# Kernel optimization log

Hardware: AMD Instinct MI355X
Metric: run time of the kernel (lower is better)

## Reference

```python
import jax, jax.numpy as jnp
import numpy as np


def setup_inputs() -> dict:
    key = jax.random.key(0)
    k0, k1 = jax.random.split(key)
    b, n, m, e = 8, 2048, 2048, 1024
    mat_0 = jax.random.normal(k0, (b, n, e), dtype=jnp.float32)
    mat_1 = jax.random.normal(k1, (b, m, e), dtype=jnp.float32)
    return {"mat_0": mat_0, "mat_1": mat_1}


def reference(mat_0, mat_1):
    # Original tiles to [b,n,m,e], multiplies, and sums over e.
    # Mathematically identical to a batched QK^T matmul: [b,n,m].
    return jnp.einsum('bne,bme->bnm', mat_0, mat_1)
```

## Files before the change

kernel.cpp:

```cpp
#include <hip/hip_runtime.h>
#include <hip/hip_bf16.h>

typedef __attribute__((ext_vector_type(8))) short short8;
typedef __attribute__((ext_vector_type(4))) float f32x4;
typedef __attribute__((ext_vector_type(4))) unsigned int u32x4;
typedef unsigned short u16;
typedef __attribute__((address_space(1))) void gvoid;
typedef __attribute__((address_space(3))) void lvoid;

static constexpr int BATCH = 8;
static constexpr int NDIM  = 2048;
static constexpr int MDIM  = 2048;
static constexpr int EDIM  = 1024;

__device__ __forceinline__ unsigned bf16rne_pair(float a, float b) {
  unsigned ua = __float_as_uint(a), ub = __float_as_uint(b);
  ua = (ua + 0x7FFFu + ((ua >> 16) & 1u)) >> 16;
  ub = (ub + 0x7FFFu + ((ub >> 16) & 1u)) >> 16;
  return ua | (ub << 16);
}

__global__ __launch_bounds__(256)
void cvt_kernel(const float* __restrict__ A, const float* __restrict__ B,
                u16* __restrict__ Abf, u16* __restrict__ Bbf) {
  const int half = (BATCH * NDIM * EDIM) / (256 * 8);
  int bid = blockIdx.x;
  const float* src; u16* dst;
  if (bid < half) { src = A; dst = Abf; }
  else            { src = B; dst = Bbf; bid -= half; }
  size_t idx = ((size_t)bid * 256 + threadIdx.x) * 8;
  f32x4 x = *(const f32x4*)(src + idx);
  f32x4 y = *(const f32x4*)(src + idx + 4);
  u32x4 r;
  r[0] = bf16rne_pair(x[0], x[1]);
  r[1] = bf16rne_pair(x[2], x[3]);
  r[2] = bf16rne_pair(y[0], y[1]);
  r[3] = bf16rne_pair(y[2], y[3]);
  *(u32x4*)(dst + idx) = r;
}

__device__ __forceinline__ void async_cp16(const void* g, void* l) {
  __builtin_amdgcn_global_load_lds((gvoid*)g, (lvoid*)l, 16, 0, 0);
}

#define BAR() do { asm volatile("" ::: "memory"); \
                   __builtin_amdgcn_s_barrier(); \
                   asm volatile("" ::: "memory"); } while (0)
#define WAITVM(N) asm volatile("s_waitcnt vmcnt(" #N ")" ::: "memory")

static constexpr int BM = 256;
static constexpr int BN = 256;
static constexpr int BK = 64;
static constexpr int KTILES = EDIM / BK;

__global__ __launch_bounds__(512, 2)
void bmm_8ph_kernel(const u16* __restrict__ A, const u16* __restrict__ B,
                    float* __restrict__ C) {
  __shared__ u16 sh[2][2][BM * BK];

  const int tid  = threadIdx.x;
  const int lane = tid & 63;
  const int wave = tid >> 6;
  const int wr   = wave >> 2;
  const int wc   = wave & 3;
  const int quad = lane >> 4;
  const int ml   = lane & 15;

  const int tcol  = blockIdx.x;
  const int trow  = blockIdx.y;
  const int batch = blockIdx.z;

  const u16* Ab = A + (size_t)batch * NDIM * EDIM + (size_t)trow * BM * EDIM;
  const u16* Bb = B + (size_t)batch * MDIM * EDIM + (size_t)tcol * BN * EDIM;

  const int r0 = tid >> 3;
  const int cs = (tid & 7) ^ (r0 & 7);
  const u16* gA = Ab + (size_t)r0 * EDIM + cs * 8;
  const u16* gB = Bb + (size_t)r0 * EDIM + cs * 8;

#define STG(buf, ab, h, gptr, t) do {                                          \
    const u16* _g = (gptr) + (size_t)((h) * 128) * EDIM + (size_t)(t) * BK;    \
    async_cp16(_g,                   &sh[buf][ab][(h) * 8192 + wave * 512]);   \
    async_cp16(_g + (size_t)64 * EDIM,                                         \
               &sh[buf][ab][(h) * 8192 + 4096 + wave * 512]);                  \
  } while (0)

  const int aBase = (wr * 128 + ml) * 64;
  const int bBase = (wc * 64 + ml) * 64;
  const int kc0 = ((quad     ) ^ (ml & 7)) * 8;
  const int kc1 = ((quad + 4 ) ^ (ml & 7)) * 8;

  short8 ar[4][2], br0[2][2], br1[2][2];
  f32x4 acc[8][4] = {};

#define LDA(buf, mh) do {                                                      \
    _Pragma("unroll")                                                          \
    for (int q = 0; q < 4; ++q) {                                              \
      ar[q][0] = *(const short8*)&sh[buf][0][aBase + (mh)*4096 + q*1024 + kc0];\
      ar[q][1] = *(const short8*)&sh[buf][0][aBase + (mh)*4096 + q*1024 + kc1];\
    } } while (0)

#define LDB(dst, buf, nh) do {                                                 \
    _Pragma("unroll")                                                          \
    for (int n = 0; n < 2; ++n) {                                              \
      dst[n][0] = *(const short8*)&sh[buf][1][bBase + (nh)*2048 + n*1024 + kc0];\
      dst[n][1] = *(const short8*)&sh[buf][1][bBase + (nh)*2048 + n*1024 + kc1];\
    } } while (0)

#define MM(mh, nh, BSRC) do {                                                  \
    __builtin_amdgcn_s_setprio(1);                                             \
    _Pragma("unroll")                                                          \
    for (int q = 0; q < 4; ++q)                                                \
      _Pragma("unroll")                                                        \
      for (int n = 0; n < 2; ++n)                                              \
        _Pragma("unroll")                                                      \
        for (int ks = 0; ks < 2; ++ks)                                         \
          acc[(mh)*4 + q][(nh)*2 + n] = __builtin_amdgcn_mfma_f32_16x16x32_bf16(\
              ar[q][ks], BSRC[n][ks], acc[(mh)*4 + q][(nh)*2 + n], 0, 0, 0);   \
    __builtin_amdgcn_s_setprio(0);                                             \
  } while (0)

  STG(0, 0, 0, gA, 0);
  STG(0, 0, 1, gA, 0);
  STG(0, 1, 0, gB, 0);
  STG(0, 1, 1, gB, 0);
  STG(1, 1, 0, gB, 1);
  STG(1, 1, 1, gB, 1);
  WAITVM(4);
  BAR();

#pragma unroll 1
  for (int i = 0; i < 7; ++i) {
    const int t1 = 2 * i + 1, p0 = 2 * i + 2, p1 = 2 * i + 3;
    LDA(0, 0); LDB(br0, 0, 0);
    STG(1, 0, 0, gA, t1);
    BAR(); MM(0, 0, br0); BAR();
    LDB(br1, 0, 1);
    STG(1, 0, 1, gA, t1);
    BAR(); MM(0, 1, br1); BAR();
    LDA(0, 1);
    STG(0, 1, 0, gB, p0);
    BAR(); MM(1, 1, br1); BAR();
    STG(0, 1, 1, gB, p0);
    WAITVM(4);
    BAR(); MM(1, 0, br0); BAR();
    LDA(1, 0); LDB(br0, 1, 0);
    STG(0, 0, 0, gA, p0);
    BAR(); MM(0, 0, br0); BAR();
    LDB(br1, 1, 1);
    STG(0, 0, 1, gA, p0);
    BAR(); MM(0, 1, br1); BAR();
    LDA(1, 1);
    STG(1, 1, 0, gB, p1);
    BAR(); MM(1, 1, br1); BAR();
    STG(1, 1, 1, gB, p1);
    WAITVM(4);
    BAR(); MM(1, 0, br0); BAR();
  }

  {
    LDA(0, 0); LDB(br0, 0, 0);
    STG(1, 0, 0, gA, 15);
    BAR(); MM(0, 0, br0); BAR();
    LDB(br1, 0, 1);
    STG(1, 0, 1, gA, 15);
    BAR(); MM(0, 1, br1); BAR();
    LDA(0, 1);
    BAR(); MM(1, 1, br1); BAR();
    WAITVM(0);
    BAR(); MM(1, 0, br0); BAR();
    LDA(1, 0); LDB(br0, 1, 0);
    BAR(); MM(0, 0, br0); BAR();
    LDB(br1, 1, 1);
    BAR(); MM(0, 1, br1); BAR();
    LDA(1, 1);
    BAR(); MM(1, 1, br1); BAR();
    MM(1, 0, br0);
  }

  float* Cb = C + (size_t)batch * NDIM * MDIM
                + (size_t)(trow * BM + wr * 128 + quad * 4) * MDIM
                + (tcol * BN + wc * 64 + ml);
#pragma unroll
  for (int mi = 0; mi < 8; ++mi) {
#pragma unroll
    for (int ni = 0; ni < 4; ++ni) {
      float* cp = Cb + (size_t)(mi * 16) * MDIM + ni * 16;
#pragma unroll
      for (int r = 0; r < 4; ++r)
        cp[(size_t)r * MDIM] = acc[mi][ni][r];
    }
  }
#undef STG
#undef LDA
#undef LDB
#undef MM
}

static constexpr int FBM = 128;
static constexpr int FBN = 128;
static constexpr int FBK = 32;
static constexpr int FKIT = EDIM / FBK;
static constexpr int LSTR = 40;

__device__ __forceinline__ unsigned pk(float lo, float hi) {
  return __builtin_amdgcn_perm(__float_as_uint(hi), __float_as_uint(lo), 0x07060302u);
}
__device__ __forceinline__ u32x4 pack8(f32x4 x, f32x4 y) {
  u32x4 r;
  r[0] = pk(x[0], x[1]); r[1] = pk(x[2], x[3]);
  r[2] = pk(y[0], y[1]); r[3] = pk(y[2], y[3]);
  return r;
}

__global__ __launch_bounds__(256, 3)
void bmm_bt_kernel(const float* __restrict__ A, const float* __restrict__ B,
                   float* __restrict__ C) {
  __shared__ u16 As[FBM * LSTR];
  __shared__ u16 Bs[FBN * LSTR];

  const int tid  = threadIdx.x;
  const int lane = tid & 63;
  const int wave = tid >> 6;
  const int quad = lane >> 4;
  const int ml   = lane & 15;
  const int wrow = (wave >> 1) * 64;
  const int wcol = (wave & 1) * 64;

  const int tcol  = blockIdx.x;
  const int trow  = blockIdx.y;
  const int batch = blockIdx.z;

  const float* Ab = A + (size_t)batch * NDIM * EDIM + (size_t)trow * FBM * EDIM;
  const float* Bb = B + (size_t)batch * MDIM * EDIM + (size_t)tcol * FBN * EDIM;
  float*       Cb = C + (size_t)batch * NDIM * MDIM;

  const int r0 = tid >> 2;
  const int p0 = (tid & 3) * 8;
  const int r1 = r0 + 64;

  const float* pA0 = Ab + (size_t)r0 * EDIM + p0;
  const float* pA1 = Ab + (size_t)r1 * EDIM + p0;
  const float* pB0 = Bb + (size_t)r0 * EDIM + p0;
  const float* pB1 = Bb + (size_t)r1 * EDIM + p0;

  u16* wA0 = &As[r0 * LSTR + p0];
  u16* wA1 = &As[r1 * LSTR + p0];
  u16* wB0 = &Bs[r0 * LSTR + p0];
  u16* wB1 = &Bs[r1 * LSTR + p0];

  f32x4 a0 = *(const f32x4*)(pA0);
  f32x4 a1 = *(const f32x4*)(pA0 + 4);
  f32x4 a2 = *(const f32x4*)(pA1);
  f32x4 a3 = *(const f32x4*)(pA1 + 4);
  f32x4 b0 = *(const f32x4*)(pB0);
  f32x4 b1 = *(const f32x4*)(pB0 + 4);
  f32x4 b2 = *(const f32x4*)(pB1);
  f32x4 b3 = *(const f32x4*)(pB1 + 4);

  f32x4 acc[4][4] = {};

  for (int kb = 0; kb < FKIT; ++kb) {
    __syncthreads();
    *(u32x4*)wA0 = pack8(a0, a1);
    *(u32x4*)wA1 = pack8(a2, a3);
    *(u32x4*)wB0 = pack8(b0, b1);
    *(u32x4*)wB1 = pack8(b2, b3);
    __syncthreads();

    if (kb + 1 < FKIT) {
      const int off = (kb + 1) * FBK;
      a0 = *(const f32x4*)(pA0 + off);
      a1 = *(const f32x4*)(pA0 + off + 4);
      a2 = *(const f32x4*)(pA1 + off);
      a3 = *(const f32x4*)(pA1 + off + 4);
      b0 = *(const f32x4*)(pB0 + off);
      b1 = *(const f32x4*)(pB0 + off + 4);
      b2 = *(const f32x4*)(pB1 + off);
      b3 = *(const f32x4*)(pB1 + off + 4);
    }

    short8 af[4], bfr[4];
#pragma unroll
    for (int i = 0; i < 4; ++i)
      af[i] = *(const short8*)&As[(wrow + i * 16 + ml) * LSTR + quad * 8];
#pragma unroll
    for (int i = 0; i < 4; ++i)
      bfr[i] = *(const short8*)&Bs[(wcol + i * 16 + ml) * LSTR + quad * 8];

#pragma unroll
    for (int mi = 0; mi < 4; ++mi)
#pragma unroll
      for (int ni = 0; ni < 4; ++ni)
        acc[mi][ni] = __builtin_amdgcn_mfma_f32_16x16x32_bf16(
            af[mi], bfr[ni], acc[mi][ni], 0, 0, 0);
  }

  const int crow = trow * FBM + wrow + quad * 4;
  const int ccol = tcol * FBN + wcol + ml;
#pragma unroll
  for (int mi = 0; mi < 4; ++mi) {
#pragma unroll
    for (int ni = 0; ni < 4; ++ni) {
      float* cp = Cb + (size_t)(crow + mi * 16) * MDIM + (ccol + ni * 16);
#pragma unroll
      for (int r = 0; r < 4; ++r)
        cp[(size_t)r * MDIM] = acc[mi][ni][r];
    }
  }
}

extern "C" void kernel_launch(void* const* d_in, const int* in_sizes, int n_in,
                              void* d_out, int out_size, void* d_ws, size_t ws_size,
                              hipStream_t stream) {
  const float* A = (const float*)d_in[0];
  const float* B = (const float*)d_in[1];
  float*       C = (float*)d_out;

  const size_t elems = (size_t)BATCH * NDIM * EDIM;
  const size_t need  = 2 * elems * sizeof(u16);

  if (ws_size >= need) {
    u16* Abf = (u16*)d_ws;
    u16* Bbf = Abf + elems;
    const int cvt_blocks = (int)(2 * elems / (256 * 8));
    cvt_kernel<<<cvt_blocks, 256, 0, stream>>>(A, B, Abf, Bbf);
    dim3 grid(MDIM / BN, NDIM / BM, BATCH);
    bmm_8ph_kernel<<<grid, dim3(512), 0, stream>>>(Abf, Bbf, C);
  } else {
    dim3 grid(MDIM / FBN, NDIM / FBM, BATCH);
    bmm_bt_kernel<<<grid, dim3(256), 0, stream>>>(A, B, C);
  }
}
```

Measured before the change: 288.9 us.

## Fuse fp32-to-bf16 conversion into GEMM staging and remap blocks for locality

Drops the separate conversion pass and its bf16 workspace. The GEMM now loads fp32 tiles from global memory into registers, packs them with the hardware bf16 convert instruction, and writes them swizzled into LDS, interleaved with the existing 8-phase MFMA schedule. It also remaps block indices so that consecutive workgroups are spread across batches and tiles. This removes a full read and write of both inputs plus one kernel launch. In exchange, each workgroup reads twice as many bytes from global memory through registers instead of async LDS loads, which raises register pressure and adds lgkm waits to every phase.

Result: slower. 525.9 us (+82.0%).

```diff
diff --git a/kernel.cpp b/kernel.cpp
--- a/kernel.cpp
+++ b/kernel.cpp
@@ -1,61 +1,26 @@
 #include <hip/hip_runtime.h>
-#include <hip/hip_bf16.h>
 
 typedef __attribute__((ext_vector_type(8))) short short8;
 typedef __attribute__((ext_vector_type(4))) float f32x4;
-typedef __attribute__((ext_vector_type(4))) unsigned int u32x4;
+typedef __attribute__((ext_vector_type(2))) unsigned int u32x2;
 typedef unsigned short u16;
-typedef __attribute__((address_space(1))) void gvoid;
-typedef __attribute__((address_space(3))) void lvoid;
 
 static constexpr int BATCH = 8;
 static constexpr int NDIM  = 2048;
 static constexpr int MDIM  = 2048;
 static constexpr int EDIM  = 1024;
-
-__device__ __forceinline__ unsigned bf16rne_pair(float a, float b) {
-  unsigned ua = __float_as_uint(a), ub = __float_as_uint(b);
-  ua = (ua + 0x7FFFu + ((ua >> 16) & 1u)) >> 16;
-  ub = (ub + 0x7FFFu + ((ub >> 16) & 1u)) >> 16;
-  return ua | (ub << 16);
-}
-
-__global__ __launch_bounds__(256)
-void cvt_kernel(const float* __restrict__ A, const float* __restrict__ B,
-                u16* __restrict__ Abf, u16* __restrict__ Bbf) {
-  const int half = (BATCH * NDIM * EDIM) / (256 * 8);
-  int bid = blockIdx.x;
-  const float* src; u16* dst;
-  if (bid < half) { src = A; dst = Abf; }
-  else            { src = B; dst = Bbf; bid -= half; }
-  size_t idx = ((size_t)bid * 256 + threadIdx.x) * 8;
-  f32x4 x = *(const f32x4*)(src + idx);
-  f32x4 y = *(const f32x4*)(src + idx + 4);
-  u32x4 r;
-  r[0] = bf16rne_pair(x[0], x[1]);
-  r[1] = bf16rne_pair(x[2], x[3]);
-  r[2] = bf16rne_pair(y[0], y[1]);
-  r[3] = bf16rne_pair(y[2], y[3]);
-  *(u32x4*)(dst + idx) = r;
-}
-
-__device__ __forceinline__ void async_cp16(const void* g, void* l) {
-  __builtin_amdgcn_global_load_lds((gvoid*)g, (lvoid*)l, 16, 0, 0);
-}
+static constexpr int BM    = 256;
+static constexpr int BN    = 256;
+static constexpr int BK    = 64;
 
 #define BAR() do { asm volatile("" ::: "memory"); \
                    __builtin_amdgcn_s_barrier(); \
                    asm volatile("" ::: "memory"); } while (0)
-#define WAITVM(N) asm volatile("s_waitcnt vmcnt(" #N ")" ::: "memory")
-
-static constexpr int BM = 256;
-static constexpr int BN = 256;
-static constexpr int BK = 64;
-static constexpr int KTILES = EDIM / BK;
+#define WFENCE() asm volatile("s_waitcnt lgkmcnt(0)" ::: "memory")
 
 __global__ __launch_bounds__(512, 2)
-void bmm_8ph_kernel(const u16* __restrict__ A, const u16* __restrict__ B,
-                    float* __restrict__ C) {
+void bmm_fused_kernel(const float* __restrict__ A, const float* __restrict__ B,
+                      float* __restrict__ C) {
   __shared__ u16 sh[2][2][BM * BK];
 
   const int tid  = threadIdx.x;
@@ -66,109 +31,139 @@
   const int quad = lane >> 4;
   const int ml   = lane & 15;
 
-  const int tcol  = blockIdx.x;
-  const int trow  = blockIdx.y;
-  const int batch = blockIdx.z;
-
-  const u16* Ab = A + (size_t)batch * NDIM * EDIM + (size_t)trow * BM * EDIM;
-  const u16* Bb = B + (size_t)batch * MDIM * EDIM + (size_t)tcol * BN * EDIM;
-
-  const int r0 = tid >> 3;
-  const int cs = (tid & 7) ^ (r0 & 7);
-  const u16* gA = Ab + (size_t)r0 * EDIM + cs * 8;
-  const u16* gB = Bb + (size_t)r0 * EDIM + cs * 8;
-
-#define STG(buf, ab, h, gptr, t) do {                                          \
-    const u16* _g = (gptr) + (size_t)((h) * 128) * EDIM + (size_t)(t) * BK;    \
-    async_cp16(_g,                   &sh[buf][ab][(h) * 8192 + wave * 512]);   \
-    async_cp16(_g + (size_t)64 * EDIM,                                         \
-               &sh[buf][ab][(h) * 8192 + 4096 + wave * 512]);                  \
-  } while (0)
+  const int flat  = (int)blockIdx.x + 8 * (int)blockIdx.y + 64 * (int)blockIdx.z;
+  const int nf    = (flat & 7) * 64 + (flat >> 3);
+  const int batch = nf >> 6;
+  const int trow  = (nf >> 3) & 7;
+  const int tcol  = nf & 7;
+
+  const float* Ab = A + (size_t)batch * NDIM * EDIM + (size_t)trow * BM * EDIM;
+  const float* Bb = B + (size_t)batch * MDIM * EDIM + (size_t)tcol * BN * EDIM;
+
+  const int rowb = tid >> 4;
+  const int colf = (tid & 15) * 4;
+  const int swzoff = ((((tid & 15) >> 1) ^ (rowb & 7)) << 3) | ((tid & 1) << 2);
+  const float* pA = Ab + (size_t)rowb * EDIM + colf;
+  const float* pB = Bb + (size_t)rowb * EDIM + colf;
 
   const int aBase = (wr * 128 + ml) * 64;
   const int bBase = (wc * 64 + ml) * 64;
-  const int kc0 = ((quad     ) ^ (ml & 7)) * 8;
-  const int kc1 = ((quad + 4 ) ^ (ml & 7)) * 8;
+  const int kc0 = ((quad    ) ^ (ml & 7)) * 8;
+  const int kc1 = ((quad + 4) ^ (ml & 7)) * 8;
 
   short8 ar[4][2], br0[2][2], br1[2][2];
   f32x4 acc[8][4] = {};
+  f32x4 s0v[4], s1v[4];
+
+#define ISS(Sp, P, h, t) do {                                                  \
+    const float* _p = (P) + (size_t)((h) * 128) * EDIM + (size_t)(t) * BK;     \
+    Sp[0] = *(const f32x4*)(_p);                                               \
+    Sp[1] = *(const f32x4*)(_p + (size_t)32 * EDIM);                           \
+    Sp[2] = *(const f32x4*)(_p + (size_t)64 * EDIM);                           \
+    Sp[3] = *(const f32x4*)(_p + (size_t)96 * EDIM);                           \
+  } while (0)
+
+#define WRT(Sp, buf, ab, h) do {                                               \
+    _Pragma("unroll")                                                          \
+    for (int _j = 0; _j < 4; ++_j) {                                           \
+      unsigned _lo, _hi;                                                       \
+      asm("v_cvt_pk_bf16_f32 %0, %1, %2"                                       \
+          : "=v"(_lo) : "v"(Sp[_j][0]), "v"(Sp[_j][1]));                       \
+      asm("v_cvt_pk_bf16_f32 %0, %1, %2"                                       \
+          : "=v"(_hi) : "v"(Sp[_j][2]), "v"(Sp[_j][3]));                       \
+      u32x2 _u; _u[0] = _lo; _u[1] = _hi;                                      \
+      *(u32x2*)&sh[buf][ab][((h) * 128 + rowb + _j * 32) * 64 + swzoff] = _u;  \
+    } } while (0)
 
 #define LDA(buf, mh) do {                                                      \
     _Pragma("unroll")                                                          \
-    for (int q = 0; q < 4; ++q) {                                              \
-      ar[q][0] = *(const short8*)&sh[buf][0][aBase + (mh)*4096 + q*1024 + kc0];\
-      ar[q][1] = *(const short8*)&sh[buf][0][aBase + (mh)*4096 + q*1024 + kc1];\
+    for (int _q = 0; _q < 4; ++_q) {                                           \
+      ar[_q][0] = *(const short8*)&sh[buf][0][aBase + (mh)*4096 + _q*1024 + kc0];\
+      ar[_q][1] = *(const short8*)&sh[buf][0][aBase + (mh)*4096 + _q*1024 + kc1];\
     } } while (0)
 
 #define LDB(dst, buf, nh) do {                                                 \
     _Pragma("unroll")                                                          \
-    for (int n = 0; n < 2; ++n) {                                              \
-      dst[n][0] = *(const short8*)&sh[buf][1][bBase + (nh)*2048 + n*1024 + kc0];\
-      dst[n][1] = *(const short8*)&sh[buf][1][bBase + (nh)*2048 + n*1024 + kc1];\
+    for (int _n = 0; _n < 2; ++_n) {                                           \
+      dst[_n][0] = *(const short8*)&sh[buf][1][bBase + (nh)*2048 + _n*1024 + kc0];\
+      dst[_n][1] = *(const short8*)&sh[buf][1][bBase + (nh)*2048 + _n*1024 + kc1];\
     } } while (0)
 
 #define MM(mh, nh, BSRC) do {                                                  \
     __builtin_amdgcn_s_setprio(1);                                             \
     _Pragma("unroll")                                                          \
-    for (int q = 0; q < 4; ++q)                                                \
+    for (int _q = 0; _q < 4; ++_q)                                             \
       _Pragma("unroll")                                                        \
-      for (int n = 0; n < 2; ++n)                                              \
+      for (int _n = 0; _n < 2; ++_n)                                           \
         _Pragma("unroll")                                                      \
-        for (int ks = 0; ks < 2; ++ks)                                         \
-          acc[(mh)*4 + q][(nh)*2 + n] = __builtin_amdgcn_mfma_f32_16x16x32_bf16(\
-              ar[q][ks], BSRC[n][ks], acc[(mh)*4 + q][(nh)*2 + n], 0, 0, 0);   \
+        for (int _ks = 0; _ks < 2; ++_ks)                                      \
+          acc[(mh)*4 + _q][(nh)*2 + _n] = __builtin_amdgcn_mfma_f32_16x16x32_bf16(\
+              ar[_q][_ks], BSRC[_n][_ks], acc[(mh)*4 + _q][(nh)*2 + _n], 0, 0, 0);\
     __builtin_amdgcn_s_setprio(0);                                             \
   } while (0)
 
-  STG(0, 0, 0, gA, 0);
-  STG(0, 0, 1, gA, 0);
-  STG(0, 1, 0, gB, 0);
-  STG(0, 1, 1, gB, 0);
-  STG(1, 1, 0, gB, 1);
-  STG(1, 1, 1, gB, 1);
-  WAITVM(4);
+  ISS(s1v, pA, 0, 0);
+  ISS(s0v, pA, 1, 0);
+  WRT(s1v, 0, 0, 0);
+  ISS(s1v, pB, 0, 0);
+  WRT(s0v, 0, 0, 1);
+  ISS(s0v, pB, 1, 0);
+  WRT(s1v, 0, 1, 0);
+  ISS(s1v, pA, 0, 1);
+  WRT(s0v, 0, 1, 1);
+  ISS(s0v, pB, 0, 1);
+  WRT(s1v, 1, 0, 0);
+  ISS(s1v, pA, 1, 1);
+  WFENCE();
   BAR();
 
 #pragma unroll 1
   for (int i = 0; i < 7; ++i) {
     const int t1 = 2 * i + 1, p0 = 2 * i + 2, p1 = 2 * i + 3;
     LDA(0, 0); LDB(br0, 0, 0);
-    STG(1, 0, 0, gA, t1);
-    BAR(); MM(0, 0, br0); BAR();
+    WRT(s1v, 1, 0, 1);
+    ISS(s1v, pB, 1, t1);
+    BAR(); MM(0, 0, br0); WFENCE(); BAR();
     LDB(br1, 0, 1);
-    STG(1, 0, 1, gA, t1);
-    BAR(); MM(0, 1, br1); BAR();
+    WRT(s0v, 1, 1, 0);
+    ISS(s0v, pA, 0, p0);
+    BAR(); MM(0, 1, br1); WFENCE(); BAR();
     LDA(0, 1);
-    STG(0, 1, 0, gB, p0);
-    BAR(); MM(1, 1, br1); BAR();
-    STG(0, 1, 1, gB, p0);
-    WAITVM(4);
-    BAR(); MM(1, 0, br0); BAR();
+    WRT(s1v, 1, 1, 1);
+    ISS(s1v, pA, 1, p0);
+    BAR(); MM(1, 1, br1); WFENCE(); BAR();
+    WRT(s0v, 0, 0, 0);
+    ISS(s0v, pB, 0, p0);
+    BAR(); MM(1, 0, br0); WFENCE(); BAR();
     LDA(1, 0); LDB(br0, 1, 0);
-    STG(0, 0, 0, gA, p0);
-    BAR(); MM(0, 0, br0); BAR();
+    WRT(s1v, 0, 0, 1);
+    ISS(s1v, pB, 1, p0);
+    BAR(); MM(0, 0, br0); WFENCE(); BAR();
     LDB(br1, 1, 1);
-    STG(0, 0, 1, gA, p0);
-    BAR(); MM(0, 1, br1); BAR();
+    WRT(s0v, 0, 1, 0);
+    ISS(s0v, pA, 0, p1);
+    BAR(); MM(0, 1, br1); WFENCE(); BAR();
     LDA(1, 1);
-    STG(1, 1, 0, gB, p1);
-    BAR(); MM(1, 1, br1); BAR();
-    STG(1, 1, 1, gB, p1);
-    WAITVM(4);
-    BAR(); MM(1, 0, br0); BAR();
+    WRT(s1v, 0, 1, 1);
+    ISS(s1v, pA, 1, p1);
+    BAR(); MM(1, 1, br1); WFENCE(); BAR();
+    WRT(s0v, 1, 0, 0);
+    ISS(s0v, pB, 0, p1);
+    BAR(); MM(1, 0, br0); WFENCE(); BAR();
   }
 
   {
     LDA(0, 0); LDB(br0, 0, 0);
-    STG(1, 0, 0, gA, 15);
-    BAR(); MM(0, 0, br0); BAR();
+    WRT(s1v, 1, 0, 1);
+    ISS(s1v, pB, 1, 15);
+    BAR(); MM(0, 0, br0); WFENCE(); BAR();
     LDB(br1, 0, 1);
-    STG(1, 0, 1, gA, 15);
-    BAR(); MM(0, 1, br1); BAR();
+    WRT(s0v, 1, 1, 0);
+    BAR(); MM(0, 1, br1); WFENCE(); BAR();
     LDA(0, 1);
-    BAR(); MM(1, 1, br1); BAR();
-    WAITVM(0);
-    BAR(); MM(1, 0, br0); BAR();
+    WRT(s1v, 1, 1, 1);
+    BAR(); MM(1, 1, br1); WFENCE(); BAR();
+    MM(1, 0, br0);
     LDA(1, 0); LDB(br0, 1, 0);
     BAR(); MM(0, 0, br0); BAR();
     LDB(br1, 1, 1);
@@ -191,123 +186,11 @@
         cp[(size_t)r * MDIM] = acc[mi][ni][r];
     }
   }
-#undef STG
+#undef ISS
+#undef WRT
 #undef LDA
 #undef LDB
 #undef MM
-}
-
-static constexpr int FBM = 128;
-static constexpr int FBN = 128;
-static constexpr int FBK = 32;
-static constexpr int FKIT = EDIM / FBK;
-static constexpr int LSTR = 40;
-
-__device__ __forceinline__ unsigned pk(float lo, float hi) {
-  return __builtin_amdgcn_perm(__float_as_uint(hi), __float_as_uint(lo), 0x07060302u);
-}
-__device__ __forceinline__ u32x4 pack8(f32x4 x, f32x4 y) {
-  u32x4 r;
-  r[0] = pk(x[0], x[1]); r[1] = pk(x[2], x[3]);
-  r[2] = pk(y[0], y[1]); r[3] = pk(y[2], y[3]);
-  return r;
-}
-
-__global__ __launch_bounds__(256, 3)
-void bmm_bt_kernel(const float* __restrict__ A, const float* __restrict__ B,
-                   float* __restrict__ C) {
-  __shared__ u16 As[FBM * LSTR];
-  __shared__ u16 Bs[FBN * LSTR];
-
-  const int tid  = threadIdx.x;
-  const int lane = tid & 63;
-  const int wave = tid >> 6;
-  const int quad = lane >> 4;
-  const int ml   = lane & 15;
-  const int wrow = (wave >> 1) * 64;
-  const int wcol = (wave & 1) * 64;
-
-  const int tcol  = blockIdx.x;
-  const int trow  = blockIdx.y;
-  const int batch = blockIdx.z;
-
-  const float* Ab = A + (size_t)batch * NDIM * EDIM + (size_t)trow * FBM * EDIM;
-  const float* Bb = B + (size_t)batch * MDIM * EDIM + (size_t)tcol * FBN * EDIM;
-  float*       Cb = C + (size_t)batch * NDIM * MDIM;
-
-  const int r0 = tid >> 2;
-  const int p0 = (tid & 3) * 8;
-  const int r1 = r0 + 64;
-
-  const float* pA0 = Ab + (size_t)r0 * EDIM + p0;
-  const float* pA1 = Ab + (size_t)r1 * EDIM + p0;
-  const float* pB0 = Bb + (size_t)r0 * EDIM + p0;
-  const float* pB1 = Bb + (size_t)r1 * EDIM + p0;
-
-  u16* wA0 = &As[r0 * LSTR + p0];
-  u16* wA1 = &As[r1 * LSTR + p0];
-  u16* wB0 = &Bs[r0 * LSTR + p0];
-  u16* wB1 = &Bs[r1 * LSTR + p0];
-
-  f32x4 a0 = *(const f32x4*)(pA0);
-  f32x4 a1 = *(const f32x4*)(pA0 + 4);
-  f32x4 a2 = *(const f32x4*)(pA1);
-  f32x4 a3 = *(const f32x4*)(pA1 + 4);
-  f32x4 b0 = *(const f32x4*)(pB0);
-  f32x4 b1 = *(const f32x4*)(pB0 + 4);
-  f32x4 b2 = *(const f32x4*)(pB1);
-  f32x4 b3 = *(const f32x4*)(pB1 + 4);
-
-  f32x4 acc[4][4] = {};
-
-  for (int kb = 0; kb < FKIT; ++kb) {
-    __syncthreads();
-    *(u32x4*)wA0 = pack8(a0, a1);
-    *(u32x4*)wA1 = pack8(a2, a3);
-    *(u32x4*)wB0 = pack8(b0, b1);
-    *(u32x4*)wB1 = pack8(b2, b3);
-    __syncthreads();
-
-    if (kb + 1 < FKIT) {
-      const int off = (kb + 1) * FBK;
-      a0 = *(const f32x4*)(pA0 + off);
-      a1 = *(const f32x4*)(pA0 + off + 4);
-      a2 = *(const f32x4*)(pA1 + off);
-      a3 = *(const f32x4*)(pA1 + off + 4);
-      b0 = *(const f32x4*)(pB0 + off);
-      b1 = *(const f32x4*)(pB0 + off + 4);
-      b2 = *(const f32x4*)(pB1 + off);
-      b3 = *(const f32x4*)(pB1 + off + 4);
-    }
-
-    short8 af[4], bfr[4];
-#pragma unroll
-    for (int i = 0; i < 4; ++i)
-      af[i] = *(const short8*)&As[(wrow + i * 16 + ml) * LSTR + quad * 8];
-#pragma unroll
-    for (int i = 0; i < 4; ++i)
-      bfr[i] = *(const short8*)&Bs[(wcol + i * 16 + ml) * LSTR + quad * 8];
-
-#pragma unroll
-    for (int mi = 0; mi < 4; ++mi)
-#pragma unroll
-      for (int ni = 0; ni < 4; ++ni)
-        acc[mi][ni] = __builtin_amdgcn_mfma_f32_16x16x32_bf16(
-            af[mi], bfr[ni], acc[mi][ni], 0, 0, 0);
-  }
-
-  const int crow = trow * FBM + wrow + quad * 4;
-  const int ccol = tcol * FBN + wcol + ml;
-#pragma unroll
-  for (int mi = 0; mi < 4; ++mi) {
-#pragma unroll
-    for (int ni = 0; ni < 4; ++ni) {
-      float* cp = Cb + (size_t)(crow + mi * 16) * MDIM + (ccol + ni * 16);
-#pragma unroll
-      for (int r = 0; r < 4; ++r)
-        cp[(size_t)r * MDIM] = acc[mi][ni][r];
-    }
-  }
 }
 
 extern "C" void kernel_launch(void* const* d_in, const int* in_sizes, int n_in,
@@ -316,19 +199,8 @@
   const float* A = (const float*)d_in[0];
   const float* B = (const float*)d_in[1];
   float*       C = (float*)d_out;
-
-  const size_t elems = (size_t)BATCH * NDIM * EDIM;
-  const size_t need  = 2 * elems * sizeof(u16);
-
-  if (ws_size >= need) {
-    u16* Abf = (u16*)d_ws;
-    u16* Bbf = Abf + elems;
-    const int cvt_blocks = (int)(2 * elems / (256 * 8));
-    cvt_kernel<<<cvt_blocks, 256, 0, stream>>>(A, B, Abf, Bbf);
-    dim3 grid(MDIM / BN, NDIM / BM, BATCH);
-    bmm_8ph_kernel<<<grid, dim3(512), 0, stream>>>(Abf, Bbf, C);
-  } else {
-    dim3 grid(MDIM / FBN, NDIM / FBM, BATCH);
-    bmm_bt_kernel<<<grid, dim3(256), 0, stream>>>(A, B, C);
-  }
+  (void)d_ws; (void)ws_size;
+
+  dim3 grid(MDIM / BN, NDIM / BM, BATCH);
+  bmm_fused_kernel<<<grid, dim3(512), 0, stream>>>(A, B, C);
 }
```
